# Optimization experiments

Hardware: AMD Instinct MI355X
Metric: run time of the kernel (lower is better)

The kernel has to match this reference:

```python
import jax, jax.numpy as jnp
import numpy as np

D = 131072   # input_dim = 2*256*256
H = 512      # lstm_hidden_dim
OUT = 128    # out_dim


def _lstm_cell(x, h, c, W_ih, W_hh, b_ih, b_hh):
    # PyTorch LSTMCell: gates in order (i, f, g, o)
    gates = x @ W_ih.T + b_ih + h @ W_hh.T + b_hh  # [1, 4H]
    i, f, g, o = jnp.split(gates, 4, axis=-1)
    i = jax.nn.sigmoid(i)
    f = jax.nn.sigmoid(f)
    g = jnp.tanh(g)
    o = jax.nn.sigmoid(o)
    c_new = f * c + i * g
    h_new = o * jnp.tanh(c_new)
    return h_new, c_new


def setup_inputs() -> dict:
    key = jax.random.key(0)
    ks = jax.random.split(key, 20)
    s_ih = 1.0 / np.sqrt(H)
    inp = {
        "dL_dU": jax.random.normal(ks[0], (256, 256), jnp.float32),
        "dL_dV": jax.random.normal(ks[1], (256, 256), jnp.float32),
        "hidden": jax.random.normal(ks[2], (2, 1, H), jnp.float32),
        "cell": jax.random.normal(ks[3], (2, 1, H), jnp.float32),
        "W_ih1": jax.random.uniform(ks[4], (4 * H, D), jnp.float32, -s_ih, s_ih),
        "W_hh1": jax.random.uniform(ks[5], (4 * H, H), jnp.float32, -s_ih, s_ih),
        "b_ih1": jax.random.uniform(ks[6], (4 * H,), jnp.float32, -s_ih, s_ih),
        "b_hh1": jax.random.uniform(ks[7], (4 * H,), jnp.float32, -s_ih, s_ih),
        "W_ih2": jax.random.uniform(ks[8], (4 * H, H), jnp.float32, -s_ih, s_ih),
        "W_hh2": jax.random.uniform(ks[9], (4 * H, H), jnp.float32, -s_ih, s_ih),
        "b_ih2": jax.random.uniform(ks[10], (4 * H,), jnp.float32, -s_ih, s_ih),
        "b_hh2": jax.random.uniform(ks[11], (4 * H,), jnp.float32, -s_ih, s_ih),
        "W1": jax.random.uniform(ks[12], (OUT * OUT, H), jnp.float32, -s_ih, s_ih),
        "b1": jax.random.uniform(ks[13], (OUT * OUT,), jnp.float32, -s_ih, s_ih),
        "W2": jax.random.uniform(ks[14], (1, H), jnp.float32, -s_ih, s_ih),
        "b2": jax.random.uniform(ks[15], (1,), jnp.float32, -s_ih, s_ih),
        "W3": jax.random.uniform(ks[16], (1, H), jnp.float32, -s_ih, s_ih),
        "b3": jax.random.uniform(ks[17], (1,), jnp.float32, -s_ih, s_ih),
    }
    return inp


def reference(dL_dU, dL_dV, hidden, cell,
              W_ih1, W_hh1, b_ih1, b_hh1,
              W_ih2, W_hh2, b_ih2, b_hh2,
              W1, b1, W2, b2, W3, b3):
    grad_flat = jnp.concatenate([dL_dU.reshape(-1), dL_dV.reshape(-1)], axis=0)[None, :]  # [1, D]
    h0, c0 = _lstm_cell(grad_flat, hidden[0], cell[0], W_ih1, W_hh1, b_ih1, b_hh1)
    h1, c1 = _lstm_cell(h0, hidden[1], cell[1], W_ih2, W_hh2, b_ih2, b_hh2)
    g = (h1 @ W1.T + b1).reshape(OUT, OUT)
    step_size = jnp.clip(h1 @ W2.T + b2, 1e-07, 0.005)
    m_c = jnp.clip(2.0 * jnp.clip(h0 @ W3.T + b3, 0.0, 1.0), 0.0, 1.0)
    return (g, step_size, m_c, jnp.stack((h0, h1)), jnp.stack((c0, c1)))
```

## Files before the change

kernel.cpp:

```cpp
#include <hip/hip_runtime.h>
#include <math.h>

#define D_IN 131072
#define H 512
#define G4 2048
#define OUTN 16384

#define OFF_STEP 16384
#define OFF_MC   16385
#define OFF_H0   16386
#define OFF_H1   16898
#define OFF_C0   17410
#define OFF_C1   17922

__device__ __forceinline__ float sigmoidf_(float x) {
    return 1.0f / (1.0f + __expf(-x));
}

__device__ __forceinline__ float dot4(float4 a, float4 b) {
    return a.x*b.x + a.y*b.y + a.z*b.z + a.w*b.w;
}

__global__ __launch_bounds__(256) void k_gemv1(
    const float* __restrict__ U, const float* __restrict__ V,
    const float* __restrict__ Wih, const float* __restrict__ Whh,
    const float* __restrict__ bih, const float* __restrict__ bhh,
    const float* __restrict__ hidden, float* __restrict__ gates)
{
    const int r = blockIdx.x;
    const int t = threadIdx.x;
    const float4* __restrict__ Wrow = (const float4*)(Wih + (size_t)r * D_IN);
    const float4* __restrict__ U4 = (const float4*)U;
    const float4* __restrict__ V4 = (const float4*)V;
    float acc = 0.0f;
    #pragma unroll 4
    for (int idx = t; idx < 16384; idx += 256) {
        acc += dot4(Wrow[idx], U4[idx]);
    }
    #pragma unroll 4
    for (int idx = t; idx < 16384; idx += 256) {
        acc += dot4(Wrow[idx + 16384], V4[idx]);
    }
    if (t < 128) {
        const float4* Wh4 = (const float4*)(Whh + (size_t)r * H);
        const float4* h4  = (const float4*)hidden;
        acc += dot4(Wh4[t], h4[t]);
    }
    #pragma unroll
    for (int off = 32; off > 0; off >>= 1) acc += __shfl_down(acc, off);
    __shared__ float s[4];
    if ((t & 63) == 0) s[t >> 6] = acc;
    __syncthreads();
    if (t == 0) {
        gates[r] = s[0] + s[1] + s[2] + s[3] + bih[r] + bhh[r];
    }
}

__global__ __launch_bounds__(1024) void k_l2fused(
    const float* __restrict__ gates1, const float* __restrict__ cell_in,
    const float* __restrict__ hidden,
    const float* __restrict__ Wih2, const float* __restrict__ Whh2,
    const float* __restrict__ bih2, const float* __restrict__ bhh2,
    const float* __restrict__ W3, const float* __restrict__ b3,
    float* __restrict__ gates2, float* __restrict__ out)
{
    __shared__ float h0s[H];
    __shared__ float red[16];
    const int tid = threadIdx.x;
    if (tid < H) {
        float ig = sigmoidf_(gates1[tid]);
        float fg = sigmoidf_(gates1[H + tid]);
        float gg = tanhf(gates1[2*H + tid]);
        float og = sigmoidf_(gates1[3*H + tid]);
        float c  = fg * cell_in[tid] + ig * gg;
        float h  = og * tanhf(c);
        h0s[tid] = h;
        if (blockIdx.x == 0) {
            out[OFF_H0 + tid] = h;
            out[OFF_C0 + tid] = c;
        }
    }
    __syncthreads();
    const int wv = tid >> 6, lane = tid & 63;
    const int row = blockIdx.x * 16 + wv;
    const float4* __restrict__ Wr = (const float4*)(Wih2 + (size_t)row * H);
    const float4* __restrict__ Hr = (const float4*)(Whh2 + (size_t)row * H);
    const float4* h4 = (const float4*)h0s;
    const float4* __restrict__ y4 = (const float4*)(hidden + H);
    float acc = dot4(Wr[lane],      h4[lane])      + dot4(Hr[lane],      y4[lane])
              + dot4(Wr[lane + 64], h4[lane + 64]) + dot4(Hr[lane + 64], y4[lane + 64]);
    #pragma unroll
    for (int off = 32; off > 0; off >>= 1) acc += __shfl_down(acc, off);
    if (lane == 0) gates2[row] = acc + bih2[row] + bhh2[row];

    if (blockIdx.x == 0) {
        float p = (tid < H) ? h0s[tid] * W3[tid] : 0.0f;
        #pragma unroll
        for (int off = 32; off > 0; off >>= 1) p += __shfl_down(p, off);
        if (lane == 0) red[wv] = p;
        __syncthreads();
        if (tid == 0) {
            float v = b3[0];
            #pragma unroll
            for (int i = 0; i < 16; ++i) v += red[i];
            v = fminf(fmaxf(v, 0.0f), 1.0f);
            out[OFF_MC] = fminf(2.0f * v, 1.0f);
        }
    }
}

__global__ __launch_bounds__(1024) void k_l3fused(
    const float* __restrict__ gates2, const float* __restrict__ cell_in,
    const float* __restrict__ W1, const float* __restrict__ b1,
    const float* __restrict__ W2, const float* __restrict__ b2,
    float* __restrict__ out)
{
    __shared__ float h1s[H];
    __shared__ float red[16];
    const int tid = threadIdx.x;
    if (tid < H) {
        float ig = sigmoidf_(gates2[tid]);
        float fg = sigmoidf_(gates2[H + tid]);
        float gg = tanhf(gates2[2*H + tid]);
        float og = sigmoidf_(gates2[3*H + tid]);
        float c  = fg * cell_in[H + tid] + ig * gg;
        float h  = og * tanhf(c);
        h1s[tid] = h;
        if (blockIdx.x == 0) {
            out[OFF_H1 + tid] = h;
            out[OFF_C1 + tid] = c;
        }
    }
    __syncthreads();
    const int wv = tid >> 6, lane = tid & 63;
    const int row = blockIdx.x * 16 + wv;
    const float4* __restrict__ Wr = (const float4*)(W1 + (size_t)row * H);
    const float4* h4 = (const float4*)h1s;
    float acc = dot4(Wr[lane], h4[lane]) + dot4(Wr[lane + 64], h4[lane + 64]);
    #pragma unroll
    for (int off = 32; off > 0; off >>= 1) acc += __shfl_down(acc, off);
    if (lane == 0) out[row] = acc + b1[row];

    if (blockIdx.x == 0) {
        float p = (tid < H) ? h1s[tid] * W2[tid] : 0.0f;
        #pragma unroll
        for (int off = 32; off > 0; off >>= 1) p += __shfl_down(p, off);
        if (lane == 0) red[wv] = p;
        __syncthreads();
        if (tid == 0) {
            float v = b2[0];
            #pragma unroll
            for (int i = 0; i < 16; ++i) v += red[i];
            out[OFF_STEP] = fminf(fmaxf(v, 1e-7f), 0.005f);
        }
    }
}

extern "C" void kernel_launch(void* const* d_in, const int* in_sizes, int n_in,
                              void* d_out, int out_size, void* d_ws, size_t ws_size,
                              hipStream_t stream) {
    const float* dL_dU  = (const float*)d_in[0];
    const float* dL_dV  = (const float*)d_in[1];
    const float* hidden = (const float*)d_in[2];
    const float* cell   = (const float*)d_in[3];
    const float* W_ih1  = (const float*)d_in[4];
    const float* W_hh1  = (const float*)d_in[5];
    const float* b_ih1  = (const float*)d_in[6];
    const float* b_hh1  = (const float*)d_in[7];
    const float* W_ih2  = (const float*)d_in[8];
    const float* W_hh2  = (const float*)d_in[9];
    const float* b_ih2  = (const float*)d_in[10];
    const float* b_hh2  = (const float*)d_in[11];
    const float* W1     = (const float*)d_in[12];
    const float* b1     = (const float*)d_in[13];
    const float* W2     = (const float*)d_in[14];
    const float* b2     = (const float*)d_in[15];
    const float* W3     = (const float*)d_in[16];
    const float* b3     = (const float*)d_in[17];

    float* out = (float*)d_out;
    float* ws  = (float*)d_ws;
    float* gates1 = ws;
    float* gates2 = ws + 2048;

    k_gemv1<<<G4, 256, 0, stream>>>(dL_dU, dL_dV, W_ih1, W_hh1, b_ih1, b_hh1,
                                    hidden, gates1);
    k_l2fused<<<G4/16, 1024, 0, stream>>>(gates1, cell, hidden,
                                          W_ih2, W_hh2, b_ih2, b_hh2,
                                          W3, b3, gates2, out);
    k_l3fused<<<OUTN/16, 1024, 0, stream>>>(gates2, cell, W1, b1, W2, b2, out);
    (void)in_sizes; (void)n_in; (void)out_size; (void)ws_size;
}
```

Measured before the change: 206.9 us.

## Stage input vector in LDS across 4 rows per block; split final LSTM cell

The first GEMV now processes four weight rows per 1024-thread block and stages 2048-float4 chunks of the input gradient vector in shared memory, so each chunk is loaded once and reused by four rows. The final stage is split: a single-block kernel computes the layer-2 cell state, h1 and step size, and a separate kernel does the output GEMV without every block recomputing the cell nonlinearities. The cost is 32 block-wide barriers in the main GEMV, which may reduce memory-level parallelism on the bandwidth-bound 1 GB weight stream, plus one extra kernel launch.

After: 220.4 us. 6.6% more time.

```diff
diff --git a/kernel.cpp b/kernel.cpp
--- a/kernel.cpp
+++ b/kernel.cpp
@@ -21,38 +21,53 @@
     return a.x*b.x + a.y*b.y + a.z*b.z + a.w*b.w;
 }
 
-__global__ __launch_bounds__(256) void k_gemv1(
+#define K1_ROWS 4
+__global__ __launch_bounds__(1024) void k_gemv1(
     const float* __restrict__ U, const float* __restrict__ V,
     const float* __restrict__ Wih, const float* __restrict__ Whh,
     const float* __restrict__ bih, const float* __restrict__ bhh,
     const float* __restrict__ hidden, float* __restrict__ gates)
 {
-    const int r = blockIdx.x;
-    const int t = threadIdx.x;
-    const float4* __restrict__ Wrow = (const float4*)(Wih + (size_t)r * D_IN);
+    __shared__ float4 xs[2048];
+    __shared__ float red[16];
+    const int tid  = threadIdx.x;
+    const int wv   = tid >> 6;
+    const int lane = tid & 63;
+    const int rloc = wv >> 2;
+    const int q    = wv & 3;
+    const int row  = blockIdx.x * K1_ROWS + rloc;
+    const float4* __restrict__ Wrow = (const float4*)(Wih + (size_t)row * D_IN);
     const float4* __restrict__ U4 = (const float4*)U;
     const float4* __restrict__ V4 = (const float4*)V;
     float acc = 0.0f;
-    #pragma unroll 4
-    for (int idx = t; idx < 16384; idx += 256) {
-        acc += dot4(Wrow[idx], U4[idx]);
-    }
-    #pragma unroll 4
-    for (int idx = t; idx < 16384; idx += 256) {
-        acc += dot4(Wrow[idx + 16384], V4[idx]);
-    }
-    if (t < 128) {
-        const float4* Wh4 = (const float4*)(Whh + (size_t)r * H);
-        const float4* h4  = (const float4*)hidden;
-        acc += dot4(Wh4[t], h4[t]);
+    for (int c = 0; c < 16; ++c) {
+        const float4* __restrict__ src = (c < 8) ? (U4 + (c << 11))
+                                                 : (V4 + ((c - 8) << 11));
+        __syncthreads();
+        xs[tid]        = src[tid];
+        xs[tid + 1024] = src[tid + 1024];
+        __syncthreads();
+        const float4* __restrict__ Wc = Wrow + (c << 11);
+        const int base = (q << 9) + lane;
+        #pragma unroll
+        for (int k = 0; k < 8; ++k) {
+            const int j = base + (k << 6);
+            acc += dot4(Wc[j], xs[j]);
+        }
+    }
+    if (q == 0) {
+        const float4* __restrict__ Wh4 = (const float4*)(Whh + (size_t)row * H);
+        const float4* h4 = (const float4*)hidden;
+        acc += dot4(Wh4[lane], h4[lane]) + dot4(Wh4[lane + 64], h4[lane + 64]);
     }
     #pragma unroll
     for (int off = 32; off > 0; off >>= 1) acc += __shfl_down(acc, off);
-    __shared__ float s[4];
-    if ((t & 63) == 0) s[t >> 6] = acc;
+    if (lane == 0) red[wv] = acc;
     __syncthreads();
-    if (t == 0) {
-        gates[r] = s[0] + s[1] + s[2] + s[3] + bih[r] + bhh[r];
+    if (tid < K1_ROWS) {
+        const int b = tid << 2;
+        const int r = blockIdx.x * K1_ROWS + tid;
+        gates[r] = red[b] + red[b+1] + red[b+2] + red[b+3] + bih[r] + bhh[r];
     }
 }
 
@@ -109,51 +124,45 @@
     }
 }
 
-__global__ __launch_bounds__(1024) void k_l3fused(
+__global__ __launch_bounds__(512) void k_cell2(
     const float* __restrict__ gates2, const float* __restrict__ cell_in,
+    const float* __restrict__ W2, const float* __restrict__ b2,
+    float* __restrict__ h1, float* __restrict__ out)
+{
+    __shared__ float s[8];
+    const int j = threadIdx.x;
+    float ig = sigmoidf_(gates2[j]);
+    float fg = sigmoidf_(gates2[H + j]);
+    float gg = tanhf(gates2[2*H + j]);
+    float og = sigmoidf_(gates2[3*H + j]);
+    float c  = fg * cell_in[H + j] + ig * gg;
+    float h  = og * tanhf(c);
+    h1[j] = h;
+    out[OFF_H1 + j] = h;
+    out[OFF_C1 + j] = c;
+    float p = h * W2[j];
+    #pragma unroll
+    for (int off = 32; off > 0; off >>= 1) p += __shfl_down(p, off);
+    if ((j & 63) == 0) s[j >> 6] = p;
+    __syncthreads();
+    if (j == 0) {
+        float v = s[0]+s[1]+s[2]+s[3]+s[4]+s[5]+s[6]+s[7] + b2[0];
+        out[OFF_STEP] = fminf(fmaxf(v, 1e-7f), 0.005f);
+    }
+}
+
+__global__ __launch_bounds__(256) void k_out_g(
     const float* __restrict__ W1, const float* __restrict__ b1,
-    const float* __restrict__ W2, const float* __restrict__ b2,
-    float* __restrict__ out)
-{
-    __shared__ float h1s[H];
-    __shared__ float red[16];
-    const int tid = threadIdx.x;
-    if (tid < H) {
-        float ig = sigmoidf_(gates2[tid]);
-        float fg = sigmoidf_(gates2[H + tid]);
-        float gg = tanhf(gates2[2*H + tid]);
-        float og = sigmoidf_(gates2[3*H + tid]);
-        float c  = fg * cell_in[H + tid] + ig * gg;
-        float h  = og * tanhf(c);
-        h1s[tid] = h;
-        if (blockIdx.x == 0) {
-            out[OFF_H1 + tid] = h;
-            out[OFF_C1 + tid] = c;
-        }
-    }
-    __syncthreads();
-    const int wv = tid >> 6, lane = tid & 63;
-    const int row = blockIdx.x * 16 + wv;
-    const float4* __restrict__ Wr = (const float4*)(W1 + (size_t)row * H);
-    const float4* h4 = (const float4*)h1s;
-    float acc = dot4(Wr[lane], h4[lane]) + dot4(Wr[lane + 64], h4[lane + 64]);
+    const float* __restrict__ h1, float* __restrict__ out)
+{
+    const int wave = (blockIdx.x * 256 + threadIdx.x) >> 6;
+    const int lane = threadIdx.x & 63;
+    const float4* __restrict__ Wr = (const float4*)(W1 + (size_t)wave * H);
+    const float4* x4 = (const float4*)h1;
+    float acc = dot4(Wr[lane], x4[lane]) + dot4(Wr[lane + 64], x4[lane + 64]);
     #pragma unroll
     for (int off = 32; off > 0; off >>= 1) acc += __shfl_down(acc, off);
-    if (lane == 0) out[row] = acc + b1[row];
-
-    if (blockIdx.x == 0) {
-        float p = (tid < H) ? h1s[tid] * W2[tid] : 0.0f;
-        #pragma unroll
-        for (int off = 32; off > 0; off >>= 1) p += __shfl_down(p, off);
-        if (lane == 0) red[wv] = p;
-        __syncthreads();
-        if (tid == 0) {
-            float v = b2[0];
-            #pragma unroll
-            for (int i = 0; i < 16; ++i) v += red[i];
-            out[OFF_STEP] = fminf(fmaxf(v, 1e-7f), 0.005f);
-        }
-    }
+    if (lane == 0) out[wave] = acc + b1[wave];
 }
 
 extern "C" void kernel_launch(void* const* d_in, const int* in_sizes, int n_in,
@@ -182,12 +191,14 @@
     float* ws  = (float*)d_ws;
     float* gates1 = ws;
     float* gates2 = ws + 2048;
-
-    k_gemv1<<<G4, 256, 0, stream>>>(dL_dU, dL_dV, W_ih1, W_hh1, b_ih1, b_hh1,
-                                    hidden, gates1);
-    k_l2fused<<<G4/16, 1024, 0, stream>>>(gates1, cell, hidden,
-                                          W_ih2, W_hh2, b_ih2, b_hh2,
-                                          W3, b3, gates2, out);
-    k_l3fused<<<OUTN/16, 1024, 0, stream>>>(gates2, cell, W1, b1, W2, b2, out);
+    float* h1     = ws + 4096;
+
+    k_gemv1<<<G4 / K1_ROWS, 1024, 0, stream>>>(dL_dU, dL_dV, W_ih1, W_hh1,
+                                               b_ih1, b_hh1, hidden, gates1);
+    k_l2fused<<<G4 / 16, 1024, 0, stream>>>(gates1, cell, hidden,
+                                            W_ih2, W_hh2, b_ih2, b_hh2,
+                                            W3, b3, gates2, out);
+    k_cell2<<<1, 512, 0, stream>>>(gates2, cell, W2, b2, h1, out);
+    k_out_g<<<OUTN / 4, 256, 0, stream>>>(W1, b1, h1, out);
     (void)in_sizes; (void)n_in; (void)out_size; (void)ws_size;
 }
```
